# Kernel optimization log

Hardware: AMD Instinct MI355X
Metric: run time of the kernel (lower is better)

Reference implementation:

```python
import jax, jax.numpy as jnp
import numpy as np

EMBED = 768
HEADS = 12
HEAD_DIM = EMBED // HEADS
FFN = 4 * EMBED
EPS = 1e-5


def setup_inputs() -> dict:
    key = jax.random.key(0)
    ks = jax.random.split(key, 12)
    s = 0.02
    inp = {
        'x': jax.random.normal(ks[0], (1, 4096, EMBED), dtype=jnp.float32),
        'Wq': jax.random.normal(ks[1], (EMBED, EMBED), dtype=jnp.float32) * s,
        'bq': jnp.zeros((EMBED,), jnp.float32),
        'Wk': jax.random.normal(ks[2], (EMBED, EMBED), dtype=jnp.float32) * s,
        'bk': jnp.zeros((EMBED,), jnp.float32),
        'Wv': jax.random.normal(ks[3], (EMBED, EMBED), dtype=jnp.float32) * s,
        'bv': jnp.zeros((EMBED,), jnp.float32),
        'Wo': jax.random.normal(ks[4], (EMBED, EMBED), dtype=jnp.float32) * s,
        'bo': jnp.zeros((EMBED,), jnp.float32),
        'ln1_g': jnp.ones((EMBED,), jnp.float32),
        'ln1_b': jnp.zeros((EMBED,), jnp.float32),
        'W1': jax.random.normal(ks[5], (EMBED, FFN), dtype=jnp.float32) * s,
        'b1': jnp.zeros((FFN,), jnp.float32),
        'W2': jax.random.normal(ks[6], (FFN, EMBED), dtype=jnp.float32) * s,
        'b2': jnp.zeros((EMBED,), jnp.float32),
        'ln2_g': jnp.ones((EMBED,), jnp.float32),
        'ln2_b': jnp.zeros((EMBED,), jnp.float32),
    }
    return inp


def _layernorm(x, g, b):
    mu = jnp.mean(x, axis=-1, keepdims=True)
    var = jnp.mean(jnp.square(x - mu), axis=-1, keepdims=True)
    return (x - mu) * jax.lax.rsqrt(var + EPS) * g + b


def reference(x, Wq, bq, Wk, bk, Wv, bv, Wo, bo, ln1_g, ln1_b, W1, b1, W2, b2, ln2_g, ln2_b):
    B, S, D = x.shape
    # QKV projections -> [B, H, S, d]
    def split_heads(t):
        return t.reshape(B, S, HEADS, HEAD_DIM).transpose(0, 2, 1, 3)
    q = split_heads(x @ Wq + bq)
    k = split_heads(x @ Wk + bk)
    v = split_heads(x @ Wv + bv)
    scores = jnp.einsum('bhqd,bhkd->bhqk', q, k) / np.sqrt(HEAD_DIM).astype(np.float32)
    attn = jax.nn.softmax(scores, axis=-1)
    ctx = jnp.einsum('bhqk,bhkd->bhqd', attn, v)
    ctx = ctx.transpose(0, 2, 1, 3).reshape(B, S, D)
    attn_out = ctx @ Wo + bo
    h = _layernorm(x + attn_out, ln1_g, ln1_b)
    ffn = jax.nn.gelu(h @ W1 + b1, approximate=False) @ W2 + b2
    return _layernorm(h + ffn, ln2_g, ln2_b)
```

## Files before the change

kernel.cpp:

```cpp
#include <hip/hip_runtime.h>
#include <hip/hip_bf16.h>

typedef __attribute__((ext_vector_type(8))) short s16x8;
typedef __attribute__((ext_vector_type(4))) int   i32x4;
typedef __attribute__((ext_vector_type(4))) float f32x4;
typedef __attribute__((ext_vector_type(8))) __bf16 bf16x8;
typedef __attribute__((ext_vector_type(4))) __bf16 bf16x4;

__device__ __forceinline__ short f2bf(float f) {
  unsigned u = __builtin_bit_cast(unsigned, f);
  u = (u + 0x7FFFu + ((u >> 16) & 1u)) >> 16;
  return (short)u;
}
__device__ __forceinline__ float bf2f(short s) {
  unsigned u = ((unsigned)(unsigned short)s) << 16;
  return __builtin_bit_cast(float, u);
}
__device__ __forceinline__ f32x4 mfma16(s16x8 a, s16x8 b, f32x4 c) {
  return __builtin_amdgcn_mfma_f32_16x16x32_bf16(
      __builtin_bit_cast(bf16x8, a), __builtin_bit_cast(bf16x8, b), c, 0, 0, 0);
}
__device__ __forceinline__ void gload16(const void* g, void* l) {
  __builtin_amdgcn_global_load_lds(
      (const __attribute__((address_space(1))) void*)g,
      (__attribute__((address_space(3))) void*)l, 16, 0, 0);
}

__global__ __launch_bounds__(256) void convert_x_kernel(const float* __restrict__ src,
                                                        short* __restrict__ dst, int n8) {
  int i = blockIdx.x * 256 + threadIdx.x;
  if (i >= n8) return;
  float4 v0 = ((const float4*)src)[i * 2];
  float4 v1 = ((const float4*)src)[i * 2 + 1];
  s16x8 o;
  o[0] = f2bf(v0.x); o[1] = f2bf(v0.y); o[2] = f2bf(v0.z); o[3] = f2bf(v0.w);
  o[4] = f2bf(v1.x); o[5] = f2bf(v1.y); o[6] = f2bf(v1.z); o[7] = f2bf(v1.w);
  *(s16x8*)&dst[i * 8] = o;
}

__global__ __launch_bounds__(256) void bconcat_kernel(const float* __restrict__ bq,
                                                      const float* __restrict__ bk,
                                                      const float* __restrict__ bv,
                                                      float* __restrict__ out) {
  int i = blockIdx.x * 256 + threadIdx.x;
  if (i < 2304) out[i] = i < 768 ? bq[i] : (i < 1536 ? bk[i - 768] : bv[i - 1536]);
}

__global__ __launch_bounds__(256) void wconv_kernel(const float* __restrict__ src,
                                                    short* __restrict__ dst, int K, int N) {
  __shared__ float t[32][33];
  int n0 = blockIdx.x * 32, k0 = blockIdx.y * 32;
  int tx = threadIdx.x & 31, ty = threadIdx.x >> 5;
#pragma unroll
  for (int r = 0; r < 4; ++r) t[ty + r * 8][tx] = src[(long)(k0 + ty + r * 8) * N + n0 + tx];
  __syncthreads();
#pragma unroll
  for (int r = 0; r < 4; ++r)
    dst[(long)(n0 + ty + r * 8) * K + k0 + tx] = f2bf(t[tx][ty + r * 8]);
}

__global__ __launch_bounds__(256) void vtrans_kernel(const short* __restrict__ qkv,
                                                     short* __restrict__ vt) {
  __shared__ short t[32][34];
  int c0 = blockIdx.x * 32, s0 = blockIdx.y * 32;
  int tx = threadIdx.x & 31, ty = threadIdx.x >> 5;
#pragma unroll
  for (int r = 0; r < 4; ++r)
    t[ty + r * 8][tx] = qkv[(long)(s0 + ty + r * 8) * 2304 + 1536 + c0 + tx];
  __syncthreads();
#pragma unroll
  for (int r = 0; r < 4; ++r)
    vt[(long)(c0 + ty + r * 8) * 4096 + s0 + tx] = t[tx][ty + r * 8];
}

template <int OUT_MODE>
__global__ __launch_bounds__(256) void gemm_kernel(const short* __restrict__ A,
                                                   const short* __restrict__ Bt,
                                                   const float* __restrict__ bias,
                                                   void* __restrict__ Cout,
                                                   int M, int N, int Kfull, int Ksub) {
  __shared__ short As[2][64 * 64];
  __shared__ short Bs[2][64 * 64];
  const int tid = threadIdx.x;
  const int wave = tid >> 6, lane = tid & 63;
  const int lr = lane & 15, lg = lane >> 4;
  const int wm = wave >> 1, wn = wave & 1;
  const int bm = blockIdx.x, bn = blockIdx.y;
  const long koff = (long)blockIdx.z * Ksub;

  f32x4 acc[4][4] = {};

  const short* Ab = A + (long)bm * 128 * Kfull + koff;
  const short* Bb = Bt + (long)bn * 128 * Kfull + koff;

  int sj[2], sr[2], skc[2];
#pragma unroll
  for (int rnd = 0; rnd < 2; ++rnd) {
    int c = tid + rnd * 256;
    int j = c >> 3, c7 = c & 7;
    int u = c7 ^ (j & 7);
    sj[rnd] = c;
    sr[rnd] = j + ((u >> 2) << 6);
    skc[rnd] = (u & 3) * 8;
  }

  auto STAGE = [&](int buf, int k0) {
#pragma unroll
    for (int rnd = 0; rnd < 2; ++rnd) {
      gload16(Ab + (long)sr[rnd] * Kfull + k0 + skc[rnd], &As[buf][sj[rnd] * 8]);
      gload16(Bb + (long)sr[rnd] * Kfull + k0 + skc[rnd], &Bs[buf][sj[rnd] * 8]);
    }
  };
  auto COMPUTE = [&](int buf) {
    s16x8 af[4], bfr[4];
#pragma unroll
    for (int m = 0; m < 4; ++m) {
      int j = m * 16 + lr;
      int c7 = ((wm << 2) | lg) ^ (lr & 7);
      af[m] = *(const s16x8*)&As[buf][j * 64 + c7 * 8];
    }
#pragma unroll
    for (int n = 0; n < 4; ++n) {
      int j = n * 16 + lr;
      int c7 = ((wn << 2) | lg) ^ (lr & 7);
      bfr[n] = *(const s16x8*)&Bs[buf][j * 64 + c7 * 8];
    }
#pragma unroll
    for (int m = 0; m < 4; ++m)
#pragma unroll
      for (int n = 0; n < 4; ++n)
        acc[m][n] = mfma16(af[m], bfr[n], acc[m][n]);
  };

  const int nt = Ksub >> 5;
  STAGE(0, 0);
  int cur = 0;
  for (int t = 0; t < nt - 1; ++t) {
    STAGE(cur ^ 1, (t + 1) * 32);
    asm volatile("s_waitcnt vmcnt(4)" ::: "memory");
    __builtin_amdgcn_s_barrier();
    __builtin_amdgcn_sched_barrier(0);
    COMPUTE(cur);
    __builtin_amdgcn_s_barrier();
    cur ^= 1;
  }
  asm volatile("s_waitcnt vmcnt(0)" ::: "memory");
  __builtin_amdgcn_s_barrier();
  __builtin_amdgcn_sched_barrier(0);
  COMPUTE(cur);

  const int gr0 = bm * 128 + wm * 64 + lg * 4;
  const int gc0 = bn * 128 + wn * 64 + lr;
  float* outF = (float*)Cout + (long)blockIdx.z * M * N;
#pragma unroll
  for (int n = 0; n < 4; ++n) {
    int col = gc0 + n * 16;
    float bb = (blockIdx.z == 0) ? bias[col] : 0.f;
#pragma unroll
    for (int m = 0; m < 4; ++m) {
#pragma unroll
      for (int j = 0; j < 4; ++j) {
        int row = gr0 + m * 16 + j;
        float v = acc[m][n][j] + bb;
        if (OUT_MODE == 2) v = 0.5f * v * (1.0f + erff(v * 0.70710678118f));
        if (OUT_MODE == 1) outF[(long)row * N + col] = v;
        else ((short*)Cout)[(long)row * N + col] = f2bf(v);
      }
    }
  }
}

__global__ __launch_bounds__(256) void flash_kernel(const short* __restrict__ qkv,
                                                    const short* __restrict__ vt,
                                                    float* __restrict__ Opart,
                                                    float* __restrict__ Lpart) {
  __shared__ short Kt[2][64 * 64];
  __shared__ short Vs[2][64 * 64];
  __shared__ short Ps[128 * 72];
  const int tid = threadIdx.x;
  const int wave = tid >> 6, lane = tid & 63;
  const int lr = lane & 15, lg = lane >> 4;
  const int lb = blockIdx.x + 32 * blockIdx.y + 384 * blockIdx.z;
  const int nlb = (lb & 7) * 96 + (lb >> 3);
  const int qb = nlb & 31;
  const int h = (nlb >> 5) % 12;
  const int sp = nlb / 384;
  const int qc = h * 64;
  const int hc = 768 + h * 64;
  const int vr = h * 64;
  const float QSCALE = 0.125f * 1.44269504088896f;

  i32x4 kr[2], vrg[2];
  auto LOADREGS = [&](int s0) {
#pragma unroll
    for (int i = 0; i < 2; ++i) {
      int c = tid + i * 256, row = c >> 3, ch = c & 7;
      kr[i] = *(const i32x4*)&qkv[(long)(s0 + row) * 2304 + hc + ch * 8];
      vrg[i] = *(const i32x4*)&vt[(long)(vr + row) * 4096 + s0 + ch * 8];
    }
  };
  auto WRITELDS = [&](int buf) {
#pragma unroll
    for (int i = 0; i < 2; ++i) {
      int c = tid + i * 256, row = c >> 3, ch = c & 7;
      int sc = ch ^ (row & 7);
      *(i32x4*)&Kt[buf][row * 64 + sc * 8] = kr[i];
      *(i32x4*)&Vs[buf][row * 64 + sc * 8] = vrg[i];
    }
  };

  const int sbase = sp * 2048;
  LOADREGS(sbase);

#pragma unroll
  for (int i = 0; i < 4; ++i) {
    int c = tid + i * 256;
    int row = c >> 3, cq = (c & 7) * 8;
    *(i32x4*)&Ps[row * 72 + cq] =
        *(const i32x4*)&qkv[(long)(qb * 128 + row) * 2304 + qc + cq];
  }
  asm volatile("s_waitcnt vmcnt(0)" ::: "memory");
  WRITELDS(0);
  LOADREGS(sbase + 64);
  asm volatile("s_waitcnt lgkmcnt(0)" ::: "memory");
  __builtin_amdgcn_s_barrier();
  __builtin_amdgcn_sched_barrier(0);

  s16x8 qf[2][2];
#pragma unroll
  for (int m = 0; m < 2; ++m)
#pragma unroll
    for (int ks = 0; ks < 2; ++ks) {
      int row = wave * 32 + m * 16 + lr;
      s16x8 v = *(const s16x8*)&Ps[row * 72 + ks * 32 + lg * 8];
#pragma unroll
      for (int e = 0; e < 8; ++e) {
        __bf16 b = (__bf16)(bf2f(v[e]) * QSCALE);
        v[e] = (short)__builtin_bit_cast(unsigned short, b);
      }
      qf[m][ks] = v;
    }

  float l_part[2] = {0.f, 0.f};
  f32x4 oacc[2][4] = {};

  int cur = 0;
  for (int it = 0; it < 32; ++it) {
    f32x4 sacc[2][4] = {};
#pragma unroll
    for (int ks = 0; ks < 2; ++ks) {
      s16x8 kf[4];
#pragma unroll
      for (int n = 0; n < 4; ++n) {
        int row = n * 16 + lr;
        int chk = (ks * 4 + lg) ^ (lr & 7);
        kf[n] = *(const s16x8*)&Kt[cur][row * 64 + chk * 8];
      }
      __builtin_amdgcn_s_setprio(1);
#pragma unroll
      for (int m = 0; m < 2; ++m)
#pragma unroll
        for (int n = 0; n < 4; ++n)
          sacc[m][n] = mfma16(kf[n], qf[m][ks], sacc[m][n]);
      __builtin_amdgcn_s_setprio(0);
    }
#pragma unroll
    for (int m = 0; m < 2; ++m) {
      const int prow = wave * 32 + m * 16 + lr;
      float rs = 0.f;
#pragma unroll
      for (int n = 0; n < 4; ++n) {
        float p0 = __builtin_amdgcn_exp2f(sacc[m][n][0]);
        float p1 = __builtin_amdgcn_exp2f(sacc[m][n][1]);
        float p2 = __builtin_amdgcn_exp2f(sacc[m][n][2]);
        float p3 = __builtin_amdgcn_exp2f(sacc[m][n][3]);
        rs += (p0 + p1) + (p2 + p3);
        bf16x4 pk;
        pk[0] = (__bf16)p0; pk[1] = (__bf16)p1;
        pk[2] = (__bf16)p2; pk[3] = (__bf16)p3;
        *(bf16x4*)&Ps[prow * 72 + n * 16 + lg * 4] = pk;
      }
      l_part[m] += rs;
    }
    if (it < 31) {
      asm volatile("s_waitcnt vmcnt(0)" ::: "memory");
      WRITELDS(cur ^ 1);
      if (it < 30) LOADREGS(sbase + (it + 2) * 64);
      __builtin_amdgcn_sched_barrier(0);
    }
#pragma unroll
    for (int ks = 0; ks < 2; ++ks) {
      s16x8 pf[2], vf[4];
#pragma unroll
      for (int m = 0; m < 2; ++m) {
        int row = wave * 32 + m * 16 + lr;
        pf[m] = *(const s16x8*)&Ps[row * 72 + ks * 32 + lg * 8];
      }
#pragma unroll
      for (int n = 0; n < 4; ++n) {
        int row = n * 16 + lr;
        int chk = (ks * 4 + lg) ^ (lr & 7);
        vf[n] = *(const s16x8*)&Vs[cur][row * 64 + chk * 8];
      }
      __builtin_amdgcn_s_setprio(1);
#pragma unroll
      for (int m = 0; m < 2; ++m)
#pragma unroll
        for (int n = 0; n < 4; ++n)
          oacc[m][n] = mfma16(pf[m], vf[n], oacc[m][n]);
      __builtin_amdgcn_s_setprio(0);
    }
    if (it < 31) {
      asm volatile("s_waitcnt lgkmcnt(0)" ::: "memory");
      __builtin_amdgcn_s_barrier();
      __builtin_amdgcn_sched_barrier(0);
      cur ^= 1;
    }
  }

  const long pbase = ((long)(h * 32 + qb) * 2 + sp) * 128;
#pragma unroll
  for (int m = 0; m < 2; ++m) {
    float l = l_part[m];
    l += __shfl_xor(l, 16);
    l += __shfl_xor(l, 32);
    if (lane < 16) Lpart[pbase + wave * 32 + m * 16 + lr] = l;
  }
#pragma unroll
  for (int m = 0; m < 2; ++m)
#pragma unroll
    for (int n = 0; n < 4; ++n)
#pragma unroll
      for (int j = 0; j < 4; ++j) {
        int row = wave * 32 + m * 16 + lg * 4 + j;
        Opart[(pbase + row) * 64 + n * 16 + lr] = oacc[m][n][j];
      }
}

__global__ __launch_bounds__(256) void combine_kernel(const float* __restrict__ Opart,
                                                      const float* __restrict__ Lpart,
                                                      short* __restrict__ ctx) {
  const int row = blockIdx.x;
  const int col = blockIdx.y * 256 + threadIdx.x;
  const int h = col >> 6, c = col & 63;
  const int qb = row >> 7, r = row & 127;
  const long p0 = ((long)(h * 32 + qb) * 2) * 128 + r;
  const long p1 = p0 + 128;
  float l = Lpart[p0] + Lpart[p1];
  float o = Opart[p0 * 64 + c] + Opart[p1 * 64 + c];
  ctx[(long)row * 768 + col] = f2bf(o / l);
}

__global__ __launch_bounds__(256) void ln_kernel(const float* __restrict__ a,
                                                 const float* __restrict__ b,
                                                 const float* __restrict__ c,
                                                 const float* __restrict__ g,
                                                 const float* __restrict__ be,
                                                 float* __restrict__ of,
                                                 short* __restrict__ ob) {
  const int row = blockIdx.x;
  const int tid = threadIdx.x;
  const long base = (long)row * 768;
  float v[3];
  float s1 = 0.f, s2 = 0.f;
#pragma unroll
  for (int kk = 0; kk < 3; ++kk) {
    int i = tid + kk * 256;
    float x = a[base + i] + b[base + i] + c[base + i];
    v[kk] = x;
    s1 += x;
    s2 += x * x;
  }
#pragma unroll
  for (int off = 1; off < 64; off <<= 1) {
    s1 += __shfl_xor(s1, off);
    s2 += __shfl_xor(s2, off);
  }
  __shared__ float ws1[4], ws2[4];
  int wave = tid >> 6;
  if ((tid & 63) == 0) { ws1[wave] = s1; ws2[wave] = s2; }
  __syncthreads();
  s1 = ws1[0] + ws1[1] + ws1[2] + ws1[3];
  s2 = ws2[0] + ws2[1] + ws2[2] + ws2[3];
  float mean = s1 * (1.f / 768.f);
  float var = s2 * (1.f / 768.f) - mean * mean;
  float rstd = rsqrtf(var + 1e-5f);
#pragma unroll
  for (int kk = 0; kk < 3; ++kk) {
    int i = tid + kk * 256;
    float o = (v[kk] - mean) * rstd * g[i] + be[i];
    if (of) of[base + i] = o;
    if (ob) ob[base + i] = f2bf(o);
  }
}

extern "C" void kernel_launch(void* const* d_in, const int* in_sizes, int n_in,
                              void* d_out, int out_size, void* d_ws, size_t ws_size,
                              hipStream_t stream) {
  const float* x   = (const float*)d_in[0];
  const float* Wq  = (const float*)d_in[1];
  const float* bq  = (const float*)d_in[2];
  const float* Wk  = (const float*)d_in[3];
  const float* bk  = (const float*)d_in[4];
  const float* Wv  = (const float*)d_in[5];
  const float* bv  = (const float*)d_in[6];
  const float* Wo  = (const float*)d_in[7];
  const float* bo  = (const float*)d_in[8];
  const float* g1  = (const float*)d_in[9];
  const float* be1 = (const float*)d_in[10];
  const float* W1  = (const float*)d_in[11];
  const float* b1  = (const float*)d_in[12];
  const float* W2  = (const float*)d_in[13];
  const float* b2  = (const float*)d_in[14];
  const float* g2  = (const float*)d_in[15];
  const float* be2 = (const float*)d_in[16];

  char* ws = (char*)d_ws;
  size_t off = 0;
  auto alloc = [&](size_t bytes) {
    char* p = ws + off;
    off += (bytes + 255) & ~(size_t)255;
    return p;
  };
  short* xb     = (short*)alloc(4096ul * 768 * 2);
  short* wqkv_t = (short*)alloc(2304ul * 768 * 2);
  short* wo_t   = (short*)alloc(768ul * 768 * 2);
  short* w1_t   = (short*)alloc(3072ul * 768 * 2);
  short* w2_t   = (short*)alloc(768ul * 3072 * 2);
  float* bqkv   = (float*)alloc(2304ul * 4);
  short* qkv    = (short*)alloc(4096ul * 2304 * 2);
  short* vt     = (short*)alloc(768ul * 4096 * 2);
  short* ctx    = (short*)alloc(4096ul * 768 * 2);
  float* attn_o = (float*)alloc(4096ul * 768 * 4);
  short* h_b    = (short*)alloc(4096ul * 768 * 2);
  float* h_f    = (float*)alloc(4096ul * 768 * 4);
  short* f1     = (short*)alloc(4096ul * 3072 * 2);
  float* Opart  = (float*)f1;
  float* Lpart  = (float*)attn_o;
  float* attn_p = (float*)qkv;
  float* ffn_p  = (float*)qkv;

  convert_x_kernel<<<1536, 256, 0, stream>>>(x, xb, 4096 * 768 / 8);
  bconcat_kernel<<<9, 256, 0, stream>>>(bq, bk, bv, bqkv);
  wconv_kernel<<<dim3(24, 24), 256, 0, stream>>>(Wq, wqkv_t, 768, 768);
  wconv_kernel<<<dim3(24, 24), 256, 0, stream>>>(Wk, wqkv_t + 768 * 768, 768, 768);
  wconv_kernel<<<dim3(24, 24), 256, 0, stream>>>(Wv, wqkv_t + 2 * 768 * 768, 768, 768);
  wconv_kernel<<<dim3(24, 24), 256, 0, stream>>>(Wo, wo_t, 768, 768);
  wconv_kernel<<<dim3(96, 24), 256, 0, stream>>>(W1, w1_t, 768, 3072);
  wconv_kernel<<<dim3(24, 96), 256, 0, stream>>>(W2, w2_t, 3072, 768);

  gemm_kernel<0><<<dim3(32, 18), 256, 0, stream>>>(xb, wqkv_t, bqkv, qkv, 4096, 2304, 768, 768);
  vtrans_kernel<<<dim3(24, 128), 256, 0, stream>>>(qkv, vt);
  flash_kernel<<<dim3(32, 12, 2), 256, 0, stream>>>(qkv, vt, Opart, Lpart);
  combine_kernel<<<dim3(4096, 3), 256, 0, stream>>>(Opart, Lpart, ctx);
  gemm_kernel<1><<<dim3(32, 6, 2), 256, 0, stream>>>(ctx, wo_t, bo, attn_p, 4096, 768, 768, 384);
  ln_kernel<<<4096, 256, 0, stream>>>(x, attn_p, attn_p + 4096ul * 768, g1, be1, h_f, h_b);
  gemm_kernel<2><<<dim3(32, 24), 256, 0, stream>>>(h_b, w1_t, b1, f1, 4096, 3072, 768, 768);
  gemm_kernel<1><<<dim3(32, 6, 2), 256, 0, stream>>>(f1, w2_t, b2, ffn_p, 4096, 768, 3072, 1536);
  ln_kernel<<<4096, 256, 0, stream>>>(h_f, ffn_p, ffn_p + 4096ul * 768, g2, be2, (float*)d_out, nullptr);
}
```

Baseline: 241.2 us.

## Restructure flash attention to split keys across waves and fuse combine

```diff
diff --git a/kernel.cpp b/kernel.cpp
--- a/kernel.cpp
+++ b/kernel.cpp
@@ -2,10 +2,10 @@
 #include <hip/hip_bf16.h>
 
 typedef __attribute__((ext_vector_type(8))) short s16x8;
+typedef __attribute__((ext_vector_type(4))) short s16x4;
 typedef __attribute__((ext_vector_type(4))) int   i32x4;
 typedef __attribute__((ext_vector_type(4))) float f32x4;
 typedef __attribute__((ext_vector_type(8))) __bf16 bf16x8;
-typedef __attribute__((ext_vector_type(4))) __bf16 bf16x4;
 
 __device__ __forceinline__ short f2bf(float f) {
   unsigned u = __builtin_bit_cast(unsigned, f);
@@ -19,6 +19,9 @@
 __device__ __forceinline__ f32x4 mfma16(s16x8 a, s16x8 b, f32x4 c) {
   return __builtin_amdgcn_mfma_f32_16x16x32_bf16(
       __builtin_bit_cast(bf16x8, a), __builtin_bit_cast(bf16x8, b), c, 0, 0, 0);
+}
+__device__ __forceinline__ f32x4 mfma16x16(s16x4 a, s16x4 b, f32x4 c) {
+  return __builtin_amdgcn_mfma_f32_16x16x16bf16_1k(a, b, c, 0, 0, 0);
 }
 __device__ __forceinline__ void gload16(const void* g, void* l) {
   __builtin_amdgcn_global_load_lds(
@@ -172,67 +175,48 @@
 
 __global__ __launch_bounds__(256) void flash_kernel(const short* __restrict__ qkv,
                                                     const short* __restrict__ vt,
-                                                    float* __restrict__ Opart,
-                                                    float* __restrict__ Lpart) {
+                                                    short* __restrict__ ctx) {
   __shared__ short Kt[2][64 * 64];
   __shared__ short Vs[2][64 * 64];
-  __shared__ short Ps[128 * 72];
+  __shared__ float Red[64 * 68];
+  __shared__ float LTab[4][64];
   const int tid = threadIdx.x;
   const int wave = tid >> 6, lane = tid & 63;
   const int lr = lane & 15, lg = lane >> 4;
-  const int lb = blockIdx.x + 32 * blockIdx.y + 384 * blockIdx.z;
+  const int lb = blockIdx.x;
   const int nlb = (lb & 7) * 96 + (lb >> 3);
-  const int qb = nlb & 31;
-  const int h = (nlb >> 5) % 12;
-  const int sp = nlb / 384;
+  const int h = nlb >> 6;
+  const int qb = nlb & 63;
   const int qc = h * 64;
   const int hc = 768 + h * 64;
   const int vr = h * 64;
   const float QSCALE = 0.125f * 1.44269504088896f;
 
-  i32x4 kr[2], vrg[2];
-  auto LOADREGS = [&](int s0) {
+  auto STAGE = [&](int buf, int it) {
+    const int s0 = it * 64;
 #pragma unroll
     for (int i = 0; i < 2; ++i) {
-      int c = tid + i * 256, row = c >> 3, ch = c & 7;
-      kr[i] = *(const i32x4*)&qkv[(long)(s0 + row) * 2304 + hc + ch * 8];
-      vrg[i] = *(const i32x4*)&vt[(long)(vr + row) * 4096 + s0 + ch * 8];
+      int c = tid + i * 256, row = c >> 3, ch = (c & 7) ^ (row & 7);
+      gload16(&qkv[(long)(s0 + row) * 2304 + hc + ch * 8], &Kt[buf][c * 8]);
+      gload16(&vt[(long)(vr + row) * 4096 + s0 + ch * 8], &Vs[buf][c * 8]);
     }
   };
-  auto WRITELDS = [&](int buf) {
-#pragma unroll
-    for (int i = 0; i < 2; ++i) {
-      int c = tid + i * 256, row = c >> 3, ch = c & 7;
-      int sc = ch ^ (row & 7);
-      *(i32x4*)&Kt[buf][row * 64 + sc * 8] = kr[i];
-      *(i32x4*)&Vs[buf][row * 64 + sc * 8] = vrg[i];
-    }
-  };
-
-  const int sbase = sp * 2048;
-  LOADREGS(sbase);
-
-#pragma unroll
-  for (int i = 0; i < 4; ++i) {
-    int c = tid + i * 256;
-    int row = c >> 3, cq = (c & 7) * 8;
-    *(i32x4*)&Ps[row * 72 + cq] =
-        *(const i32x4*)&qkv[(long)(qb * 128 + row) * 2304 + qc + cq];
+
+#pragma unroll
+  for (int i = 0; i < 2; ++i) {
+    int c = tid + i * 256, row = c >> 3, ch = (c & 7) ^ (row & 7);
+    gload16(&qkv[(long)(qb * 64 + row) * 2304 + qc + ch * 8], &Kt[0][c * 8]);
   }
   asm volatile("s_waitcnt vmcnt(0)" ::: "memory");
-  WRITELDS(0);
-  LOADREGS(sbase + 64);
-  asm volatile("s_waitcnt lgkmcnt(0)" ::: "memory");
   __builtin_amdgcn_s_barrier();
-  __builtin_amdgcn_sched_barrier(0);
-
-  s16x8 qf[2][2];
-#pragma unroll
-  for (int m = 0; m < 2; ++m)
+  s16x8 qf[4][2];
+#pragma unroll
+  for (int m = 0; m < 4; ++m)
 #pragma unroll
     for (int ks = 0; ks < 2; ++ks) {
-      int row = wave * 32 + m * 16 + lr;
-      s16x8 v = *(const s16x8*)&Ps[row * 72 + ks * 32 + lg * 8];
+      int row = m * 16 + lr;
+      int chq = (ks * 4 + lg) ^ (lr & 7);
+      s16x8 v = *(const s16x8*)&Kt[0][row * 64 + chq * 8];
 #pragma unroll
       for (int e = 0; e < 8; ++e) {
         __bf16 b = (__bf16)(bf2f(v[e]) * QSCALE);
@@ -240,120 +224,144 @@
       }
       qf[m][ks] = v;
     }
-
-  float l_part[2] = {0.f, 0.f};
-  f32x4 oacc[2][4] = {};
-
+  __syncthreads();
+
+  float l_part[4] = {0.f, 0.f, 0.f, 0.f};
+  f32x4 oacc[4][4] = {};
+
+  STAGE(0, 0);
   int cur = 0;
-  for (int it = 0; it < 32; ++it) {
-    f32x4 sacc[2][4] = {};
+  for (int it = 0; it < 64; ++it) {
+    if (it < 63) {
+      STAGE(cur ^ 1, it + 1);
+      asm volatile("s_waitcnt vmcnt(4)" ::: "memory");
+    } else {
+      asm volatile("s_waitcnt vmcnt(0)" ::: "memory");
+    }
+    __builtin_amdgcn_s_barrier();
+    __builtin_amdgcn_sched_barrier(0);
+
+    s16x8 kf[2];
 #pragma unroll
     for (int ks = 0; ks < 2; ++ks) {
-      s16x8 kf[4];
-#pragma unroll
-      for (int n = 0; n < 4; ++n) {
-        int row = n * 16 + lr;
-        int chk = (ks * 4 + lg) ^ (lr & 7);
-        kf[n] = *(const s16x8*)&Kt[cur][row * 64 + chk * 8];
-      }
-      __builtin_amdgcn_s_setprio(1);
-#pragma unroll
-      for (int m = 0; m < 2; ++m)
-#pragma unroll
-        for (int n = 0; n < 4; ++n)
-          sacc[m][n] = mfma16(kf[n], qf[m][ks], sacc[m][n]);
-      __builtin_amdgcn_s_setprio(0);
-    }
-#pragma unroll
-    for (int m = 0; m < 2; ++m) {
-      const int prow = wave * 32 + m * 16 + lr;
-      float rs = 0.f;
-#pragma unroll
-      for (int n = 0; n < 4; ++n) {
-        float p0 = __builtin_amdgcn_exp2f(sacc[m][n][0]);
-        float p1 = __builtin_amdgcn_exp2f(sacc[m][n][1]);
-        float p2 = __builtin_amdgcn_exp2f(sacc[m][n][2]);
-        float p3 = __builtin_amdgcn_exp2f(sacc[m][n][3]);
-        rs += (p0 + p1) + (p2 + p3);
-        bf16x4 pk;
-        pk[0] = (__bf16)p0; pk[1] = (__bf16)p1;
-        pk[2] = (__bf16)p2; pk[3] = (__bf16)p3;
-        *(bf16x4*)&Ps[prow * 72 + n * 16 + lg * 4] = pk;
-      }
-      l_part[m] += rs;
-    }
-    if (it < 31) {
-      asm volatile("s_waitcnt vmcnt(0)" ::: "memory");
-      WRITELDS(cur ^ 1);
-      if (it < 30) LOADREGS(sbase + (it + 2) * 64);
-      __builtin_amdgcn_sched_barrier(0);
-    }
-#pragma unroll
-    for (int ks = 0; ks < 2; ++ks) {
-      s16x8 pf[2], vf[4];
-#pragma unroll
-      for (int m = 0; m < 2; ++m) {
-        int row = wave * 32 + m * 16 + lr;
-        pf[m] = *(const s16x8*)&Ps[row * 72 + ks * 32 + lg * 8];
-      }
-#pragma unroll
-      for (int n = 0; n < 4; ++n) {
-        int row = n * 16 + lr;
-        int chk = (ks * 4 + lg) ^ (lr & 7);
-        vf[n] = *(const s16x8*)&Vs[cur][row * 64 + chk * 8];
-      }
-      __builtin_amdgcn_s_setprio(1);
-#pragma unroll
-      for (int m = 0; m < 2; ++m)
-#pragma unroll
-        for (int n = 0; n < 4; ++n)
-          oacc[m][n] = mfma16(pf[m], vf[n], oacc[m][n]);
-      __builtin_amdgcn_s_setprio(0);
-    }
-    if (it < 31) {
-      asm volatile("s_waitcnt lgkmcnt(0)" ::: "memory");
-      __builtin_amdgcn_s_barrier();
-      __builtin_amdgcn_sched_barrier(0);
-      cur ^= 1;
-    }
-  }
-
-  const long pbase = ((long)(h * 32 + qb) * 2 + sp) * 128;
-#pragma unroll
-  for (int m = 0; m < 2; ++m) {
+      int row = wave * 16 + lr;
+      int chk = (ks * 4 + lg) ^ (lr & 7);
+      kf[ks] = *(const s16x8*)&Kt[cur][row * 64 + chk * 8];
+    }
+    f32x4 sacc[4] = {};
+    __builtin_amdgcn_s_setprio(1);
+#pragma unroll
+    for (int m = 0; m < 4; ++m)
+#pragma unroll
+      for (int ks = 0; ks < 2; ++ks)
+        sacc[m] = mfma16(kf[ks], qf[m][ks], sacc[m]);
+    __builtin_amdgcn_s_setprio(0);
+
+    s16x4 pa[4];
+#pragma unroll
+    for (int m = 0; m < 4; ++m) {
+      float p0 = __builtin_amdgcn_exp2f(sacc[m][0]);
+      float p1 = __builtin_amdgcn_exp2f(sacc[m][1]);
+      float p2 = __builtin_amdgcn_exp2f(sacc[m][2]);
+      float p3 = __builtin_amdgcn_exp2f(sacc[m][3]);
+      l_part[m] += (p0 + p1) + (p2 + p3);
+      s16x4 pk;
+      pk[0] = (short)__builtin_bit_cast(unsigned short, (__bf16)p0);
+      pk[1] = (short)__builtin_bit_cast(unsigned short, (__bf16)p1);
+      pk[2] = (short)__builtin_bit_cast(unsigned short, (__bf16)p2);
+      pk[3] = (short)__builtin_bit_cast(unsigned short, (__bf16)p3);
+      pa[m] = pk;
+    }
+
+    s16x4 vf[4];
+#pragma unroll
+    for (int n = 0; n < 4; ++n) {
+      int row = n * 16 + lr;
+      int chv = (2 * wave + (lg >> 1)) ^ (lr & 7);
+      vf[n] = *(const s16x4*)&Vs[cur][row * 64 + chv * 8 + (lg & 1) * 4];
+    }
+    __builtin_amdgcn_s_setprio(1);
+#pragma unroll
+    for (int m = 0; m < 4; ++m)
+#pragma unroll
+      for (int n = 0; n < 4; ++n)
+        oacc[m][n] = mfma16x16(pa[m], vf[n], oacc[m][n]);
+    __builtin_amdgcn_s_setprio(0);
+
+    __builtin_amdgcn_s_barrier();
+    cur ^= 1;
+  }
+
+#pragma unroll
+  for (int m = 0; m < 4; ++m) {
     float l = l_part[m];
     l += __shfl_xor(l, 16);
     l += __shfl_xor(l, 32);
-    if (lane < 16) Lpart[pbase + wave * 32 + m * 16 + lr] = l;
-  }
-#pragma unroll
-  for (int m = 0; m < 2; ++m)
-#pragma unroll
-    for (int n = 0; n < 4; ++n)
-#pragma unroll
-      for (int j = 0; j < 4; ++j) {
-        int row = wave * 32 + m * 16 + lg * 4 + j;
-        Opart[(pbase + row) * 64 + n * 16 + lr] = oacc[m][n][j];
+    if (lane < 16) LTab[wave][m * 16 + lr] = l;
+  }
+  __syncthreads();
+
+  if (wave == 0) {
+#pragma unroll
+    for (int m = 0; m < 4; ++m)
+#pragma unroll
+      for (int n = 0; n < 4; ++n)
+        *(f32x4*)&Red[(n * 16 + lr) * 68 + m * 16 + lg * 4] = oacc[m][n];
+  }
+  __syncthreads();
+  if (wave == 1) {
+#pragma unroll
+    for (int m = 0; m < 4; ++m)
+#pragma unroll
+      for (int n = 0; n < 4; ++n) {
+        f32x4 r = *(const f32x4*)&Red[(n * 16 + lr) * 68 + m * 16 + lg * 4];
+        *(f32x4*)&Red[(n * 16 + lr) * 68 + m * 16 + lg * 4] = r + oacc[m][n];
       }
-}
-
-__global__ __launch_bounds__(256) void combine_kernel(const float* __restrict__ Opart,
-                                                      const float* __restrict__ Lpart,
-                                                      short* __restrict__ ctx) {
-  const int row = blockIdx.x;
-  const int col = blockIdx.y * 256 + threadIdx.x;
-  const int h = col >> 6, c = col & 63;
-  const int qb = row >> 7, r = row & 127;
-  const long p0 = ((long)(h * 32 + qb) * 2) * 128 + r;
-  const long p1 = p0 + 128;
-  float l = Lpart[p0] + Lpart[p1];
-  float o = Opart[p0 * 64 + c] + Opart[p1 * 64 + c];
-  ctx[(long)row * 768 + col] = f2bf(o / l);
+  }
+  __syncthreads();
+  if (wave == 2) {
+#pragma unroll
+    for (int m = 0; m < 4; ++m)
+#pragma unroll
+      for (int n = 0; n < 4; ++n) {
+        f32x4 r = *(const f32x4*)&Red[(n * 16 + lr) * 68 + m * 16 + lg * 4];
+        *(f32x4*)&Red[(n * 16 + lr) * 68 + m * 16 + lg * 4] = r + oacc[m][n];
+      }
+  }
+  __syncthreads();
+  if (wave == 3) {
+#pragma unroll
+    for (int m = 0; m < 4; ++m)
+#pragma unroll
+      for (int n = 0; n < 4; ++n) {
+        f32x4 r = *(const f32x4*)&Red[(n * 16 + lr) * 68 + m * 16 + lg * 4];
+        *(f32x4*)&Red[(n * 16 + lr) * 68 + m * 16 + lg * 4] = r + oacc[m][n];
+      }
+  }
+  __syncthreads();
+
+  {
+    const int q = tid >> 2, dc = (tid & 3) * 16;
+    float l = LTab[0][q] + LTab[1][q] + LTab[2][q] + LTab[3][q];
+    float rl = 1.f / l;
+    i32x4 o0, o1;
+#pragma unroll
+    for (int dd = 0; dd < 4; ++dd) {
+      int lo0 = (unsigned short)f2bf(Red[(dc + 2 * dd) * 68 + q] * rl);
+      int hi0 = (unsigned short)f2bf(Red[(dc + 2 * dd + 1) * 68 + q] * rl);
+      o0[dd] = lo0 | (hi0 << 16);
+      int lo1 = (unsigned short)f2bf(Red[(dc + 8 + 2 * dd) * 68 + q] * rl);
+      int hi1 = (unsigned short)f2bf(Red[(dc + 8 + 2 * dd + 1) * 68 + q] * rl);
+      o1[dd] = lo1 | (hi1 << 16);
+    }
+    long base = (long)(qb * 64 + q) * 768 + h * 64 + dc;
+    *(i32x4*)&ctx[base] = o0;
+    *(i32x4*)&ctx[base + 8] = o1;
+  }
 }
 
 __global__ __launch_bounds__(256) void ln_kernel(const float* __restrict__ a,
-                                                 const float* __restrict__ b,
-                                                 const float* __restrict__ c,
+                                                 const float* __restrict__ parts, int np,
                                                  const float* __restrict__ g,
                                                  const float* __restrict__ be,
                                                  float* __restrict__ of,
@@ -361,12 +369,14 @@
   const int row = blockIdx.x;
   const int tid = threadIdx.x;
   const long base = (long)row * 768;
+  const long pstride = 4096l * 768;
   float v[3];
   float s1 = 0.f, s2 = 0.f;
 #pragma unroll
   for (int kk = 0; kk < 3; ++kk) {
     int i = tid + kk * 256;
-    float x = a[base + i] + b[base + i] + c[base + i];
+    float x = a[base + i];
+    for (int z = 0; z < np; ++z) x += parts[z * pstride + base + i];
     v[kk] = x;
     s1 += x;
     s2 += x * x;
@@ -435,8 +445,6 @@
   short* h_b    = (short*)alloc(4096ul * 768 * 2);
   float* h_f    = (float*)alloc(4096ul * 768 * 4);
   short* f1     = (short*)alloc(4096ul * 3072 * 2);
-  float* Opart  = (float*)f1;
-  float* Lpart  = (float*)attn_o;
   float* attn_p = (float*)qkv;
   float* ffn_p  = (float*)qkv;
 
@@ -451,11 +459,10 @@
 
   gemm_kernel<0><<<dim3(32, 18), 256, 0, stream>>>(xb, wqkv_t, bqkv, qkv, 4096, 2304, 768, 768);
   vtrans_kernel<<<dim3(24, 128), 256, 0, stream>>>(qkv, vt);
-  flash_kernel<<<dim3(32, 12, 2), 256, 0, stream>>>(qkv, vt, Opart, Lpart);
-  combine_kernel<<<dim3(4096, 3), 256, 0, stream>>>(Opart, Lpart, ctx);
+  flash_kernel<<<768, 256, 0, stream>>>(qkv, vt, ctx);
   gemm_kernel<1><<<dim3(32, 6, 2), 256, 0, stream>>>(ctx, wo_t, bo, attn_p, 4096, 768, 768, 384);
-  ln_kernel<<<4096, 256, 0, stream>>>(x, attn_p, attn_p + 4096ul * 768, g1, be1, h_f, h_b);
+  ln_kernel<<<4096, 256, 0, stream>>>(x, attn_p, 2, g1, be1, h_f, h_b);
   gemm_kernel<2><<<dim3(32, 24), 256, 0, stream>>>(h_b, w1_t, b1, f1, 4096, 3072, 768, 768);
-  gemm_kernel<1><<<dim3(32, 6, 2), 256, 0, stream>>>(f1, w2_t, b2, ffn_p, 4096, 768, 3072, 1536);
-  ln_kernel<<<4096, 256, 0, stream>>>(h_f, ffn_p, ffn_p + 4096ul * 768, g2, be2, (float*)d_out, nullptr);
-}
+  gemm_kernel<1><<<dim3(32, 6, 4), 256, 0, stream>>>(f1, w2_t, b2, ffn_p, 4096, 768, 3072, 768);
+  ln_kernel<<<4096, 256, 0, stream>>>(h_f, ffn_p, 4, g2, be2, (float*)d_out, nullptr);
+}
```

Result: slower. 286.9 us (+19.0%).

## Merge prep kernels into one launch and write V transposed from QKV GEMM

Applied to the files above, without the earlier changes.

```diff
diff --git a/kernel.cpp b/kernel.cpp
--- a/kernel.cpp
+++ b/kernel.cpp
@@ -2,6 +2,7 @@
 #include <hip/hip_bf16.h>
 
 typedef __attribute__((ext_vector_type(8))) short s16x8;
+typedef __attribute__((ext_vector_type(4))) short s16x4;
 typedef __attribute__((ext_vector_type(4))) int   i32x4;
 typedef __attribute__((ext_vector_type(4))) float f32x4;
 typedef __attribute__((ext_vector_type(8))) __bf16 bf16x8;
@@ -26,51 +27,52 @@
       (__attribute__((address_space(3))) void*)l, 16, 0, 0);
 }
 
-__global__ __launch_bounds__(256) void convert_x_kernel(const float* __restrict__ src,
-                                                        short* __restrict__ dst, int n8) {
-  int i = blockIdx.x * 256 + threadIdx.x;
-  if (i >= n8) return;
-  float4 v0 = ((const float4*)src)[i * 2];
-  float4 v1 = ((const float4*)src)[i * 2 + 1];
-  s16x8 o;
-  o[0] = f2bf(v0.x); o[1] = f2bf(v0.y); o[2] = f2bf(v0.z); o[3] = f2bf(v0.w);
-  o[4] = f2bf(v1.x); o[5] = f2bf(v1.y); o[6] = f2bf(v1.z); o[7] = f2bf(v1.w);
-  *(s16x8*)&dst[i * 8] = o;
-}
-
-__global__ __launch_bounds__(256) void bconcat_kernel(const float* __restrict__ bq,
-                                                      const float* __restrict__ bk,
-                                                      const float* __restrict__ bv,
-                                                      float* __restrict__ out) {
-  int i = blockIdx.x * 256 + threadIdx.x;
-  if (i < 2304) out[i] = i < 768 ? bq[i] : (i < 1536 ? bk[i - 768] : bv[i - 1536]);
-}
-
-__global__ __launch_bounds__(256) void wconv_kernel(const float* __restrict__ src,
-                                                    short* __restrict__ dst, int K, int N) {
+__global__ __launch_bounds__(256) void prep_kernel(
+    const float* __restrict__ x, short* __restrict__ xb,
+    const float* __restrict__ bq, const float* __restrict__ bk,
+    const float* __restrict__ bv, float* __restrict__ bqkv,
+    const float* __restrict__ Wq, const float* __restrict__ Wk,
+    const float* __restrict__ Wv, const float* __restrict__ Wo,
+    const float* __restrict__ W1, const float* __restrict__ W2,
+    short* __restrict__ wqkv_t, short* __restrict__ wo_t,
+    short* __restrict__ w1_t, short* __restrict__ w2_t) {
   __shared__ float t[32][33];
-  int n0 = blockIdx.x * 32, k0 = blockIdx.y * 32;
-  int tx = threadIdx.x & 31, ty = threadIdx.x >> 5;
+  const int b = blockIdx.x, tid = threadIdx.x;
+  if (b < 1536) {
+    int i = b * 256 + tid;
+    float4 v0 = ((const float4*)x)[i * 2];
+    float4 v1 = ((const float4*)x)[i * 2 + 1];
+    s16x8 o;
+    o[0] = f2bf(v0.x); o[1] = f2bf(v0.y); o[2] = f2bf(v0.z); o[3] = f2bf(v0.w);
+    o[4] = f2bf(v1.x); o[5] = f2bf(v1.y); o[6] = f2bf(v1.z); o[7] = f2bf(v1.w);
+    *(s16x8*)&xb[i * 8] = o;
+    return;
+  }
+  if (b < 1545) {
+    int i = (b - 1536) * 256 + tid;
+    if (i < 2304) bqkv[i] = i < 768 ? bq[i] : (i < 1536 ? bk[i - 768] : bv[i - 1536]);
+    return;
+  }
+  const float* src; short* dst; int K, N, bx, by;
+  if (b < 3849) {
+    int t4 = b - 1545, wi = t4 / 576, r = t4 % 576;
+    bx = r % 24; by = r / 24; K = 768; N = 768;
+    src = wi == 0 ? Wq : wi == 1 ? Wk : wi == 2 ? Wv : Wo;
+    dst = wi == 0 ? wqkv_t : wi == 1 ? wqkv_t + 768 * 768
+        : wi == 2 ? wqkv_t + 2 * 768 * 768 : wo_t;
+  } else if (b < 6153) {
+    int r = b - 3849; bx = r % 96; by = r / 96; K = 768; N = 3072; src = W1; dst = w1_t;
+  } else {
+    int r = b - 6153; bx = r % 24; by = r / 24; K = 3072; N = 768; src = W2; dst = w2_t;
+  }
+  int n0 = bx * 32, k0 = by * 32;
+  int tx = tid & 31, ty = tid >> 5;
 #pragma unroll
   for (int r = 0; r < 4; ++r) t[ty + r * 8][tx] = src[(long)(k0 + ty + r * 8) * N + n0 + tx];
   __syncthreads();
 #pragma unroll
   for (int r = 0; r < 4; ++r)
     dst[(long)(n0 + ty + r * 8) * K + k0 + tx] = f2bf(t[tx][ty + r * 8]);
-}
-
-__global__ __launch_bounds__(256) void vtrans_kernel(const short* __restrict__ qkv,
-                                                     short* __restrict__ vt) {
-  __shared__ short t[32][34];
-  int c0 = blockIdx.x * 32, s0 = blockIdx.y * 32;
-  int tx = threadIdx.x & 31, ty = threadIdx.x >> 5;
-#pragma unroll
-  for (int r = 0; r < 4; ++r)
-    t[ty + r * 8][tx] = qkv[(long)(s0 + ty + r * 8) * 2304 + 1536 + c0 + tx];
-  __syncthreads();
-#pragma unroll
-  for (int r = 0; r < 4; ++r)
-    vt[(long)(c0 + ty + r * 8) * 4096 + s0 + tx] = t[tx][ty + r * 8];
 }
 
 template <int OUT_MODE>
@@ -78,6 +80,7 @@
                                                    const short* __restrict__ Bt,
                                                    const float* __restrict__ bias,
                                                    void* __restrict__ Cout,
+                                                   short* __restrict__ vtout,
                                                    int M, int N, int Kfull, int Ksub) {
   __shared__ short As[2][64 * 64];
   __shared__ short Bs[2][64 * 64];
@@ -151,6 +154,21 @@
 
   const int gr0 = bm * 128 + wm * 64 + lg * 4;
   const int gc0 = bn * 128 + wn * 64 + lr;
+  if (OUT_MODE == 0 && vtout != nullptr && bn >= 12) {
+#pragma unroll
+    for (int n = 0; n < 4; ++n) {
+      int col = gc0 + n * 16;
+      float bb = bias[col];
+#pragma unroll
+      for (int m = 0; m < 4; ++m) {
+        s16x4 pk;
+#pragma unroll
+        for (int j = 0; j < 4; ++j) pk[j] = f2bf(acc[m][n][j] + bb);
+        *(s16x4*)&vtout[(long)(col - 1536) * 4096 + gr0 + m * 16] = pk;
+      }
+    }
+    return;
+  }
   float* outF = (float*)Cout + (long)blockIdx.z * M * N;
 #pragma unroll
   for (int n = 0; n < 4; ++n) {
@@ -440,22 +458,20 @@
   float* attn_p = (float*)qkv;
   float* ffn_p  = (float*)qkv;
 
-  convert_x_kernel<<<1536, 256, 0, stream>>>(x, xb, 4096 * 768 / 8);
-  bconcat_kernel<<<9, 256, 0, stream>>>(bq, bk, bv, bqkv);
-  wconv_kernel<<<dim3(24, 24), 256, 0, stream>>>(Wq, wqkv_t, 768, 768);
-  wconv_kernel<<<dim3(24, 24), 256, 0, stream>>>(Wk, wqkv_t + 768 * 768, 768, 768);
-  wconv_kernel<<<dim3(24, 24), 256, 0, stream>>>(Wv, wqkv_t + 2 * 768 * 768, 768, 768);
-  wconv_kernel<<<dim3(24, 24), 256, 0, stream>>>(Wo, wo_t, 768, 768);
-  wconv_kernel<<<dim3(96, 24), 256, 0, stream>>>(W1, w1_t, 768, 3072);
-  wconv_kernel<<<dim3(24, 96), 256, 0, stream>>>(W2, w2_t, 3072, 768);
-
-  gemm_kernel<0><<<dim3(32, 18), 256, 0, stream>>>(xb, wqkv_t, bqkv, qkv, 4096, 2304, 768, 768);
-  vtrans_kernel<<<dim3(24, 128), 256, 0, stream>>>(qkv, vt);
+  prep_kernel<<<8457, 256, 0, stream>>>(x, xb, bq, bk, bv, bqkv,
+                                        Wq, Wk, Wv, Wo, W1, W2,
+                                        wqkv_t, wo_t, w1_t, w2_t);
+  gemm_kernel<0><<<dim3(32, 18), 256, 0, stream>>>(xb, wqkv_t, bqkv, qkv, vt,
+                                                   4096, 2304, 768, 768);
   flash_kernel<<<dim3(32, 12, 2), 256, 0, stream>>>(qkv, vt, Opart, Lpart);
   combine_kernel<<<dim3(4096, 3), 256, 0, stream>>>(Opart, Lpart, ctx);
-  gemm_kernel<1><<<dim3(32, 6, 2), 256, 0, stream>>>(ctx, wo_t, bo, attn_p, 4096, 768, 768, 384);
+  gemm_kernel<1><<<dim3(32, 6, 2), 256, 0, stream>>>(ctx, wo_t, bo, attn_p, nullptr,
+                                                     4096, 768, 768, 384);
   ln_kernel<<<4096, 256, 0, stream>>>(x, attn_p, attn_p + 4096ul * 768, g1, be1, h_f, h_b);
-  gemm_kernel<2><<<dim3(32, 24), 256, 0, stream>>>(h_b, w1_t, b1, f1, 4096, 3072, 768, 768);
-  gemm_kernel<1><<<dim3(32, 6, 2), 256, 0, stream>>>(f1, w2_t, b2, ffn_p, 4096, 768, 3072, 1536);
-  ln_kernel<<<4096, 256, 0, stream>>>(h_f, ffn_p, ffn_p + 4096ul * 768, g2, be2, (float*)d_out, nullptr);
-}
+  gemm_kernel<2><<<dim3(32, 24), 256, 0, stream>>>(h_b, w1_t, b1, f1, nullptr,
+                                                   4096, 3072, 768, 768);
+  gemm_kernel<1><<<dim3(32, 6, 2), 256, 0, stream>>>(f1, w2_t, b2, ffn_p, nullptr,
+                                                     4096, 768, 3072, 1536);
+  ln_kernel<<<4096, 256, 0, stream>>>(h_f, ffn_p, ffn_p + 4096ul * 768, g2, be2,
+                                      (float*)d_out, nullptr);
+}
```

Result: faster. 223.8 us (-7.2%).
